# Kernel optimization log

Measured on AMD Instinct MI355X. Metric: run time of the kernel, lower is better.

## Reference

```python
import jax, jax.numpy as jnp
from jax import lax
import numpy as np

B, S, E = 512, 128, 300
NF = 100          # filters per kernel size
NUM_CLASSES = 5


def setup_inputs() -> dict:
    key = jax.random.key(0)
    ks = jax.random.split(key, 9)
    def w(k, shape, fan_in):
        bound = 1.0 / np.sqrt(fan_in)
        return jax.random.uniform(k, shape, jnp.float32, -bound, bound)
    return {
        "x":   jax.random.normal(ks[0], (B, 1, S, E), jnp.float32),
        # conv weights: [out_ch=NF, in_ch=1, kh, kw=E] (the 100 separate 1-channel
        # convs of each kernel size are stacked into one grouped weight tensor)
        "w3": w(ks[1], (NF, 1, 3, E), 3 * E),
        "b3": w(ks[2], (NF,), 3 * E),
        "w4": w(ks[3], (NF, 1, 4, E), 4 * E),
        "b4": w(ks[4], (NF,), 4 * E),
        "w5": w(ks[5], (NF, 1, 5, E), 5 * E),
        "b5": w(ks[6], (NF,), 5 * E),
        "Wfc": w(ks[7], (NUM_CLASSES, 3 * NF), 3 * NF),
        "bfc": w(ks[8], (NUM_CLASSES,), 3 * NF),
    }


def _branch(x, w, b, pad):
    # conv over [B,1,S,E] with kernel [NF,1,k,E]; width fully consumed -> out [B,NF,S',1]
    y = lax.conv_general_dilated(
        x, w, window_strides=(1, 1), padding=[(pad, pad), (0, 0)],
        dimension_numbers=("NCHW", "OIHW", "NCHW"))
    y = jax.nn.relu(y + b[None, :, None, None])
    # relu then global max-pool over the length dim == max over (S', 1)
    return jnp.max(y, axis=(2, 3))  # [B, NF]


def reference(x, w3, b3, w4, b4, w5, b5, Wfc, bfc):
    feats = jnp.concatenate(
        [_branch(x, w3, b3, 0),   # k=3, no padding
         _branch(x, w4, b4, 1),   # k=4, padding (1,0)
         _branch(x, w5, b5, 2)],  # k=5, padding (2,0)
        axis=1)                   # [B, 300]
    logits = feats @ Wfc.T + bfc  # dropout is identity in eval mode
    return jax.nn.log_softmax(logits, axis=1)
```

## Files before the change

### kernel.cpp

```cpp
#include <hip/hip_runtime.h>

typedef __bf16 bf16x8 __attribute__((ext_vector_type(8)));
typedef float  f32x4  __attribute__((ext_vector_type(4)));
typedef unsigned short u16;

#define NB    512
#define SEQ   128
#define EMB   300
#define NT_TOT 19
#define KT_TOT 50
#define KT_BYTES (NT_TOT * 1024)
#define WU_ELEMS (304 * 1600)
#define OFF_FEATS (WU_ELEMS * 2)

#define AROW 640
#define A_BYTES (69 * AROW)

__device__ __forceinline__ u16 f2bf(float f) {
  unsigned u = __builtin_bit_cast(unsigned, f);
  return (u16)((u + 0x7fffu + ((u >> 16) & 1u)) >> 16);
}

__global__ void prep_weights(const float* __restrict__ w3, const float* __restrict__ w4,
                             const float* __restrict__ w5, u16* __restrict__ wu) {
  int idx = blockIdx.x * blockDim.x + threadIdx.x;
  if (idx >= WU_ELEMS) return;
  int j = idx & 7, l = (idx >> 3) & 63, t = idx >> 9;
  int nt = t % NT_TOT, kt = t / NT_TOT;
  int f  = nt * 16 + (l & 15);
  int kk = kt * 32 + ((l >> 4) << 3) + j;
  int dk = kk / 320, e = kk - dk * 320;
  float v = 0.f;
  if (f < 300 && e < 300) {
    if (f < 100)      { if (dk >= 2) v = w3[(f * 3 + dk - 2) * 300 + e]; }
    else if (f < 200) { if (dk >= 1) v = w4[((f - 100) * 4 + dk - 1) * 300 + e]; }
    else              {              v = w5[((f - 200) * 5 + dk) * 300 + e]; }
  }
  wu[idx] = f2bf(v);
}

template<int NTW>
__device__ __forceinline__ void kloop_epi(const char* xs, const char* wB,
                                          int ntb, int l, int b, int s0,
                                          const float* __restrict__ b3,
                                          const float* __restrict__ b4,
                                          const float* __restrict__ b5,
                                          float* __restrict__ feats) {
  const int lo = l & 15, hi = l >> 4;

  f32x4 acc[4][NTW];
  #pragma unroll
  for (int mt = 0; mt < 4; ++mt)
    #pragma unroll
    for (int j = 0; j < NTW; ++j) acc[mt][j] = (f32x4){0.f, 0.f, 0.f, 0.f};

  bf16x8 aC[4], aN[4], bC[NTW], bN[NTW];

  const char* gB = wB + ntb * 1024 + l * 16;
  #pragma unroll
  for (int j = 0; j < NTW; ++j) bC[j] = *reinterpret_cast<const bf16x8*>(gB + j * 1024);
  #pragma unroll
  for (int j = 0; j < NTW; ++j) bN[j] = *reinterpret_cast<const bf16x8*>(gB + KT_BYTES + j * 1024);
  gB += 2 * KT_BYTES;

  int abase[4];
  #pragma unroll
  for (int mt = 0; mt < 4; ++mt) abase[mt] = (mt * 16 + lo) * AROW + hi * 16;

  {
    const int sw = (lo & 7) << 4;
    #pragma unroll
    for (int mt = 0; mt < 4; ++mt)
      aC[mt] = *reinterpret_cast<const bf16x8*>(xs + (abase[mt] ^ sw));
  }

#define STEP(AOFF, SW, Acon, Anex, Bcon) {                                     \
    _Pragma("unroll") for (int mt = 0; mt < 4; ++mt)                           \
      Anex[mt] = *reinterpret_cast<const bf16x8*>(xs + ((abase[mt] + (AOFF)) ^ (SW))); \
    __builtin_amdgcn_s_setprio(1);                                             \
    _Pragma("unroll") for (int mt = 0; mt < 4; ++mt)                           \
    _Pragma("unroll") for (int j = 0; j < NTW; ++j)                            \
      acc[mt][j] = __builtin_amdgcn_mfma_f32_16x16x32_bf16(Acon[mt], Bcon[j],  \
                                                           acc[mt][j], 0, 0, 0); \
    __builtin_amdgcn_s_setprio(0);                                             \
    _Pragma("unroll") for (int j = 0; j < NTW; ++j)                            \
      Bcon[j] = *reinterpret_cast<const bf16x8*>(gB + j * 1024);               \
    gB += KT_BYTES; }

  #pragma unroll 1
  for (int dk = 0; dk < 5; ++dk) {
    const int sw0 = ((lo + dk) & 7) << 4;
    const int sw1 = ((lo + dk + 1) & 7) << 4;
    STEP( 64, sw0, aC, aN, bC)
    STEP(128, sw0, aN, aC, bN)
    STEP(192, sw0, aC, aN, bC)
    STEP(256, sw0, aN, aC, bN)
    STEP(320, sw0, aC, aN, bC)
    STEP(384, sw0, aN, aC, bN)
    STEP(448, sw0, aC, aN, bC)
    STEP(512, sw0, aN, aC, bN)
    STEP(576, sw0, aC, aN, bC)
    STEP(640, sw1, aN, aC, bN)
    #pragma unroll
    for (int mt = 0; mt < 4; ++mt) abase[mt] += AROW;
  }
#undef STEP

  #pragma unroll
  for (int j = 0; j < NTW; ++j) {
    int f = (ntb + j) * 16 + lo;
    if (f < 300) {
      float bia  = (f < 100) ? b3[f] : (f < 200) ? b4[f - 100] : b5[f - 200];
      int   sval = (f < 100) ? 126   : (f < 200) ? 127         : 128;
      float cmax = 0.f;
      #pragma unroll
      for (int mt = 0; mt < 4; ++mt)
        #pragma unroll
        for (int ii = 0; ii < 4; ++ii) {
          int s = s0 + mt * 16 + hi * 4 + ii;
          float v = acc[mt][j][ii] + bia;
          if (s < sval) cmax = fmaxf(cmax, v);
        }
      cmax = fmaxf(cmax, __shfl_xor(cmax, 16));
      cmax = fmaxf(cmax, __shfl_xor(cmax, 32));
      if (hi == 0)
        atomicMax((int*)&feats[b * 300 + f], __float_as_int(fmaxf(cmax, 0.f)));
    }
  }
}

__global__ __launch_bounds__(256, 3)
void conv_max_kernel(const float* __restrict__ x, const u16* __restrict__ wu,
                     const float* __restrict__ b3, const float* __restrict__ b4,
                     const float* __restrict__ b5, float* __restrict__ feats) {
  __shared__ __align__(16) char xs[A_BYTES];
  const int bid = blockIdx.x;
  const int b = bid >> 1, s0 = (bid & 1) * 64;
  const int tid = threadIdx.x;
  const int l = tid & 63, w = tid >> 6;
  const float* xb = x + (size_t)b * (SEQ * EMB);
  const char*  wB = (const char*)wu;

  for (int t = tid; t < 68 * 80; t += 256) {
    int r = t / 80, cg = t - r * 80;
    int xr = s0 - 2 + r;
    float4 v = make_float4(0.f, 0.f, 0.f, 0.f);
    if (xr >= 0 && xr < SEQ && cg < 75)
      v = *reinterpret_cast<const float4*>(xb + xr * EMB + cg * 4);
    ushort4 h;
    h.x = f2bf(v.x); h.y = f2bf(v.y); h.z = f2bf(v.z); h.w = f2bf(v.w);
    int boff = (r * AROW + cg * 8) ^ ((r & 7) << 4);
    *reinterpret_cast<ushort4*>(xs + boff) = h;
  }
  __syncthreads();

  if (w == 3) kloop_epi<4>(xs, wB, 15, l, b, s0, b3, b4, b5, feats);
  else        kloop_epi<5>(xs, wB, w * 5, l, b, s0, b3, b4, b5, feats);
}

__global__ void fc_kernel(const float* __restrict__ feats, const float* __restrict__ Wfc,
                          const float* __restrict__ bfc, float* __restrict__ out) {
  const int b = blockIdx.x, l = threadIdx.x;
  float acc[5] = {0.f, 0.f, 0.f, 0.f, 0.f};
  for (int e = l; e < 300; e += 64) {
    float fv = feats[b * 300 + e];
    #pragma unroll
    for (int c = 0; c < 5; ++c) acc[c] += fv * Wfc[c * 300 + e];
  }
  #pragma unroll
  for (int off = 32; off; off >>= 1) {
    #pragma unroll
    for (int c = 0; c < 5; ++c) acc[c] += __shfl_down(acc[c], off);
  }
  if (l == 0) {
    float lg[5], m = -1e30f;
    #pragma unroll
    for (int c = 0; c < 5; ++c) { lg[c] = acc[c] + bfc[c]; m = fmaxf(m, lg[c]); }
    float se = 0.f;
    #pragma unroll
    for (int c = 0; c < 5; ++c) se += expf(lg[c] - m);
    float ls = logf(se);
    #pragma unroll
    for (int c = 0; c < 5; ++c) out[b * 5 + c] = lg[c] - m - ls;
  }
}

extern "C" void kernel_launch(void* const* d_in, const int* in_sizes, int n_in,
                              void* d_out, int out_size, void* d_ws, size_t ws_size,
                              hipStream_t stream) {
  const float* x   = (const float*)d_in[0];
  const float* w3  = (const float*)d_in[1];
  const float* b3  = (const float*)d_in[2];
  const float* w4  = (const float*)d_in[3];
  const float* b4  = (const float*)d_in[4];
  const float* w5  = (const float*)d_in[5];
  const float* b5  = (const float*)d_in[6];
  const float* Wfc = (const float*)d_in[7];
  const float* bfc = (const float*)d_in[8];
  float* out = (float*)d_out;

  u16*   wu    = (u16*)d_ws;
  float* feats = (float*)((char*)d_ws + OFF_FEATS);

  hipMemsetAsync(feats, 0, NB * 300 * sizeof(float), stream);

  prep_weights<<<(WU_ELEMS + 255) / 256, 256, 0, stream>>>(w3, w4, w5, wu);
  conv_max_kernel<<<NB * 2, 256, 0, stream>>>(x, wu, b3, b4, b5, feats);
  fc_kernel<<<NB, 64, 0, stream>>>(feats, Wfc, bfc, out);
}
```

Measured before the change: 77.15 us.

## Regroup packed weights per wave for contiguous B loads; drop A double-buffer

The weight packing kernel now writes each wave's filter-tile group into its own contiguous region, ordered by k-tile, so each wave streams B fragments linearly instead of striding across all 19 n-tiles. The conv kernel points each wave at its group base. The A-operand LDS double buffering and the s_setprio hints are removed, so LDS reads feed the MFMAs directly. Because of that, LDS latency may be exposed before each MFMA block, in exchange for fewer registers and better global-load locality.

```diff
diff --git a/kernel.cpp b/kernel.cpp
--- a/kernel.cpp
+++ b/kernel.cpp
@@ -9,9 +9,10 @@
 #define EMB   300
 #define NT_TOT 19
 #define KT_TOT 50
-#define KT_BYTES (NT_TOT * 1024)
 #define WU_ELEMS (304 * 1600)
 #define OFF_FEATS (WU_ELEMS * 2)
+
+#define GRP_ELEMS 128000
 
 #define AROW 640
 #define A_BYTES (69 * AROW)
@@ -36,11 +37,14 @@
     else if (f < 200) { if (dk >= 1) v = w4[((f - 100) * 4 + dk - 1) * 300 + e]; }
     else              {              v = w5[((f - 200) * 5 + dk) * 300 + e]; }
   }
-  wu[idx] = f2bf(v);
+  int g    = nt / 5;
+  int tloc = nt - g * 5;
+  int ntw  = (g == 3) ? 4 : 5;
+  wu[g * GRP_ELEMS + (kt * ntw + tloc) * 512 + (l << 3) + j] = f2bf(v);
 }
 
 template<int NTW>
-__device__ __forceinline__ void kloop_epi(const char* xs, const char* wB,
+__device__ __forceinline__ void kloop_epi(const char* xs, const char* gB0,
                                           int ntb, int l, int b, int s0,
                                           const float* __restrict__ b3,
                                           const float* __restrict__ b4,
@@ -54,53 +58,43 @@
     #pragma unroll
     for (int j = 0; j < NTW; ++j) acc[mt][j] = (f32x4){0.f, 0.f, 0.f, 0.f};
 
-  bf16x8 aC[4], aN[4], bC[NTW], bN[NTW];
-
-  const char* gB = wB + ntb * 1024 + l * 16;
+  bf16x8 aa[4], bC[NTW], bN[NTW];
+
+  const char* gB = gB0 + l * 16;
   #pragma unroll
   for (int j = 0; j < NTW; ++j) bC[j] = *reinterpret_cast<const bf16x8*>(gB + j * 1024);
   #pragma unroll
-  for (int j = 0; j < NTW; ++j) bN[j] = *reinterpret_cast<const bf16x8*>(gB + KT_BYTES + j * 1024);
-  gB += 2 * KT_BYTES;
+  for (int j = 0; j < NTW; ++j) bN[j] = *reinterpret_cast<const bf16x8*>(gB + (NTW + j) * 1024);
+  gB += 2 * NTW * 1024;
 
   int abase[4];
   #pragma unroll
   for (int mt = 0; mt < 4; ++mt) abase[mt] = (mt * 16 + lo) * AROW + hi * 16;
 
-  {
-    const int sw = (lo & 7) << 4;
-    #pragma unroll
-    for (int mt = 0; mt < 4; ++mt)
-      aC[mt] = *reinterpret_cast<const bf16x8*>(xs + (abase[mt] ^ sw));
-  }
-
-#define STEP(AOFF, SW, Acon, Anex, Bcon) {                                     \
+#define STEP(AOFF, SW, Bcon) {                                                 \
     _Pragma("unroll") for (int mt = 0; mt < 4; ++mt)                           \
-      Anex[mt] = *reinterpret_cast<const bf16x8*>(xs + ((abase[mt] + (AOFF)) ^ (SW))); \
-    __builtin_amdgcn_s_setprio(1);                                             \
+      aa[mt] = *reinterpret_cast<const bf16x8*>(xs + ((abase[mt] + (AOFF)) ^ (SW))); \
     _Pragma("unroll") for (int mt = 0; mt < 4; ++mt)                           \
     _Pragma("unroll") for (int j = 0; j < NTW; ++j)                            \
-      acc[mt][j] = __builtin_amdgcn_mfma_f32_16x16x32_bf16(Acon[mt], Bcon[j],  \
+      acc[mt][j] = __builtin_amdgcn_mfma_f32_16x16x32_bf16(aa[mt], Bcon[j],    \
                                                            acc[mt][j], 0, 0, 0); \
-    __builtin_amdgcn_s_setprio(0);                                             \
     _Pragma("unroll") for (int j = 0; j < NTW; ++j)                            \
       Bcon[j] = *reinterpret_cast<const bf16x8*>(gB + j * 1024);               \
-    gB += KT_BYTES; }
+    gB += NTW * 1024; }
 
   #pragma unroll 1
   for (int dk = 0; dk < 5; ++dk) {
-    const int sw0 = ((lo + dk) & 7) << 4;
-    const int sw1 = ((lo + dk + 1) & 7) << 4;
-    STEP( 64, sw0, aC, aN, bC)
-    STEP(128, sw0, aN, aC, bN)
-    STEP(192, sw0, aC, aN, bC)
-    STEP(256, sw0, aN, aC, bN)
-    STEP(320, sw0, aC, aN, bC)
-    STEP(384, sw0, aN, aC, bN)
-    STEP(448, sw0, aC, aN, bC)
-    STEP(512, sw0, aN, aC, bN)
-    STEP(576, sw0, aC, aN, bC)
-    STEP(640, sw1, aN, aC, bN)
+    const int sw = ((lo + dk) & 7) << 4;
+    STEP(  0, sw, bC)
+    STEP( 64, sw, bN)
+    STEP(128, sw, bC)
+    STEP(192, sw, bN)
+    STEP(256, sw, bC)
+    STEP(320, sw, bN)
+    STEP(384, sw, bC)
+    STEP(448, sw, bN)
+    STEP(512, sw, bC)
+    STEP(576, sw, bN)
     #pragma unroll
     for (int mt = 0; mt < 4; ++mt) abase[mt] += AROW;
   }
@@ -139,7 +133,7 @@
   const int tid = threadIdx.x;
   const int l = tid & 63, w = tid >> 6;
   const float* xb = x + (size_t)b * (SEQ * EMB);
-  const char*  wB = (const char*)wu;
+  const char*  wB = (const char*)wu + w * (GRP_ELEMS * 2);
 
   for (int t = tid; t < 68 * 80; t += 256) {
     int r = t / 80, cg = t - r * 80;
```

New measurement: 81.00 us. 5.0% more time.
